# Kernel tuning notes

Measured on AMD Instinct MI355X. Metric: run time of the kernel, lower is better.

Reference implementation:

```python
import jax, jax.numpy as jnp
import numpy as np

ALPHA = 0.99   # config.alpha_grape
GAMMA = 0.999  # config.gamma
LAMBD = 0.7    # config.lambd_grape
T, A = 262144, 64


def setup_inputs() -> dict:
    key = jax.random.key(0)
    ks = jax.random.split(key, 7)
    q = jax.random.normal(ks[0], (T + 1, A), jnp.float32)
    q_tar = jax.random.normal(ks[1], (T + 1, A), jnp.float32)
    # pi / mu are probability distributions over actions (softmax of logits)
    pi = jax.nn.softmax(jax.random.normal(ks[2], (T + 1, A), jnp.float32), axis=-1)
    mu_t = jax.nn.softmax(jax.random.normal(ks[3], (T, A), jnp.float32), axis=-1)
    a_t = jax.random.randint(ks[4], (T,), 0, A, dtype=jnp.int32)
    r_t = jax.random.normal(ks[5], (T,), jnp.float32)
    done_t = jax.random.randint(ks[6], (T,), 0, 2, dtype=jnp.int32)
    return dict(q=q, q_tar=q_tar, pi=pi, a_t=a_t, r_t=r_t, mu_t=mu_t, done_t=done_t)


def reference(q, q_tar, pi, a_t, r_t, mu_t, done_t):
    # GRAPE.compute_targets
    l = q.shape[0] - 1
    idx = jnp.arange(l)
    pi_t, pi_tp1 = pi[:-1], pi[1:]
    q_t, q_tp1 = q[:-1], q_tar[1:]
    q_t_a = q_t[idx, a_t]                              # [T]
    v_t = jnp.sum(pi_t * q_t, axis=1)                  # [T]
    v_tp1 = jnp.sum(pi_tp1 * q_tp1, axis=1)            # [T]
    done_f = done_t.astype(q.dtype)
    q_t_a_est = r_t + (1.0 - done_f) * GAMMA * v_tp1
    td_error = q_t_a_est - q_t_a
    rho_t_a = pi_t[idx, a_t] / mu_t[idx, a_t]
    c_t_a = LAMBD * jnp.clip(rho_t_a, 0.0, 1.0)

    # backward-in-time first-order recurrence over y'
    def step(y_prime, xs):
        est, td, rho, c, d = xs
        y = jnp.where(d > 0.5, 0.0, y_prime)           # reset at episode end
        g = est + y
        y_new = LAMBD * GAMMA * rho * td + GAMMA * c * y
        return y_new, g

    _, g_q = jax.lax.scan(
        step, jnp.float32(0.0),
        (q_t_a_est, td_error, rho_t_a, c_t_a, done_f),
        reverse=True,
    )
    targets_q = g_q + ALPHA * (q_t_a - v_t)            # [T]
    advantages = (1.0 - ALPHA) * (q_t - v_t[:, None])  # [T, A]
    return targets_q, advantages
```

## Files before the change

### kernel.cpp

```cpp
#include <hip/hip_runtime.h>

#define GAMMA 0.999f
#define LAMBD 0.7f
#define ALPHA 0.99f

constexpr int A_DIM = 64;
constexpr int CH    = 128;
constexpr int BLK   = 128;

__global__ __launch_bounds__(BLK, 8)
void k_main(const float* __restrict__ q, const float* __restrict__ q_tar,
            const float* __restrict__ pi, const int* __restrict__ a_t,
            const float* __restrict__ r_t, const float* __restrict__ mu_t,
            const int* __restrict__ done_t,
            float* __restrict__ adv_out,
            float2* __restrict__ comb, float2* __restrict__ cab)
{
    __shared__ float sQa[CH], sRho[CH], sKm[CH], sRt[CH];
    __shared__ float sV[CH], sVp[CH];
    __shared__ float sWA[2], sWB[2];

    const int tid  = threadIdx.x;
    const int wave = tid >> 6, lane = tid & 63;
    const int sub  = lane >> 4, li = lane & 15;
    const int R0   = blockIdx.x * CH;

    {
        int r = R0 + tid;
        int a = a_t[r];
        sRt[tid] = r_t[r];
        sKm[tid] = 1.0f - (float)done_t[r];
        float qa = q[r * A_DIM + a];
        float pa = pi[r * A_DIM + a];
        float ma = mu_t[r * A_DIM + a];
        sQa[tid]  = qa;
        sRho[tid] = pa / ma;
    }

    #pragma unroll 2
    for (int i = 0; i < 8; ++i) {
        int lrowA = wave * 64 + i * 8 + sub;
        int lrowB = lrowA + 4;
        int gA = (R0 + lrowA) * A_DIM + li * 4;
        int gB = (R0 + lrowB) * A_DIM + li * 4;

        float4 piA  = *(const float4*)&pi[gA];
        float4 qA   = *(const float4*)&q[gA];
        float4 pipA = *(const float4*)&pi[gA + A_DIM];
        float4 qpA  = *(const float4*)&q_tar[gA + A_DIM];
        float4 piB  = *(const float4*)&pi[gB];
        float4 qB   = *(const float4*)&q[gB];
        float4 pipB = *(const float4*)&pi[gB + A_DIM];
        float4 qpB  = *(const float4*)&q_tar[gB + A_DIM];

        float s0A = piA.x*qA.x + piA.y*qA.y + piA.z*qA.z + piA.w*qA.w;
        float s1A = pipA.x*qpA.x + pipA.y*qpA.y + pipA.z*qpA.z + pipA.w*qpA.w;
        float s0B = piB.x*qB.x + piB.y*qB.y + piB.z*qB.z + piB.w*qB.w;
        float s1B = pipB.x*qpB.x + pipB.y*qpB.y + pipB.z*qpB.z + pipB.w*qpB.w;
        #pragma unroll
        for (int off = 1; off < 16; off <<= 1) {
            s0A += __shfl_xor(s0A, off);
            s1A += __shfl_xor(s1A, off);
            s0B += __shfl_xor(s0B, off);
            s1B += __shfl_xor(s1B, off);
        }

        float4 advA, advB;
        advA.x = (1.0f - ALPHA) * (qA.x - s0A);
        advA.y = (1.0f - ALPHA) * (qA.y - s0A);
        advA.z = (1.0f - ALPHA) * (qA.z - s0A);
        advA.w = (1.0f - ALPHA) * (qA.w - s0A);
        advB.x = (1.0f - ALPHA) * (qB.x - s0B);
        advB.y = (1.0f - ALPHA) * (qB.y - s0B);
        advB.z = (1.0f - ALPHA) * (qB.z - s0B);
        advB.w = (1.0f - ALPHA) * (qB.w - s0B);
        *(float4*)&adv_out[gA] = advA;
        *(float4*)&adv_out[gB] = advB;

        if (li == 0) {
            sV[lrowA] = s0A;  sVp[lrowA] = s1A;
            sV[lrowB] = s0B;  sVp[lrowB] = s1B;
        }
    }
    __syncthreads();

    float s0    = sV[tid],  s1 = sVp[tid];
    float kmask = sKm[tid];
    float qa    = sQa[tid];
    float rho   = sRho[tid];
    float est = sRt[tid] + kmask * (GAMMA * s1);
    float td  = est - qa;
    float c   = LAMBD * fminf(fmaxf(rho, 0.0f), 1.0f);
    float Fa  = (LAMBD * GAMMA) * rho * td;
    float Fb  = kmask * (GAMMA * c);
    float E   = est + ALPHA * (qa - s0);

    float Ai = Fa, Bi = Fb;
    #pragma unroll
    for (int off = 1; off < 64; off <<= 1) {
        float An = __shfl_down(Ai, off);
        float Bn = __shfl_down(Bi, off);
        if (lane + off < 64) { Ai += Bi * An; Bi *= Bn; }
    }
    if (lane == 0) { sWA[wave] = Ai; sWB[wave] = Bi; }
    float Xa = __shfl_down(Ai, 1);
    float Xb = __shfl_down(Bi, 1);
    if (lane == 63) { Xa = 0.0f; Xb = 1.0f; }
    __syncthreads();
    if (wave == 0) {
        float W1a = sWA[1], W1b = sWB[1];
        Xa = Xa + Xb * W1a;
        Xb = Xb * W1b;
    }
    comb[R0 + tid] = make_float2(E + kmask * Xa, kmask * Xb);
    if (tid == 0) {
        float W1a = sWA[1], W1b = sWB[1];
        cab[blockIdx.x] = make_float2(Ai + Bi * W1a, Bi * W1b);
    }
}

__global__ __launch_bounds__(BLK, 8)
void k_fin(const float2* __restrict__ comb, const float2* __restrict__ cab,
           float* __restrict__ targets, int nch)
{
    __shared__ float sXa[BLK], sXb[BLK];
    __shared__ float sWA[2], sWB[2];
    __shared__ float sYe;
    const int tid = threadIdx.x, bid = blockIdx.x;
    const int wave = tid >> 6, lane = tid & 63;

    const float4* cab4 = (const float4*)cab;
    float A = 0.0f, B = 1.0f;
    #pragma unroll
    for (int j = 0; j < 8; ++j) {
        float4 u = cab4[tid * 8 + j];
        A += B * u.x; B *= u.y;
        A += B * u.z; B *= u.w;
    }

    float Ai = A, Bi = B;
    #pragma unroll
    for (int off = 1; off < 64; off <<= 1) {
        float An = __shfl_down(Ai, off);
        float Bn = __shfl_down(Bi, off);
        if (lane + off < 64) { Ai += Bi * An; Bi *= Bn; }
    }
    if (lane == 0) { sWA[wave] = Ai; sWB[wave] = Bi; }
    float Xa = __shfl_down(Ai, 1);
    float Xb = __shfl_down(Bi, 1);
    if (lane == 63) { Xa = 0.0f; Xb = 1.0f; }
    __syncthreads();
    if (wave == 0) {
        Xa = Xa + Xb * sWA[1];
        Xb = Xb * sWB[1];
    }
    sXa[tid] = Xa; sXb[tid] = Xb;
    __syncthreads();

    if (tid == 0) {
        int c1 = bid + 1;
        float ye;
        if (c1 >= nch) {
            ye = 0.0f;
        } else {
            int jq = c1 >> 4, rq = c1 & 15;
            float Aa = sXa[jq], Bb = sXb[jq];
            for (int k2 = 16 * jq + 15; k2 >= c1; --k2) {
                float2 cv = cab[k2];
                Aa = cv.x + cv.y * Aa;
                Bb = cv.y * Bb;
            }
            ye = Aa;
        }
        sYe = ye;
    }
    __syncthreads();

    float2 uw = comb[bid * CH + tid];
    targets[bid * CH + tid] = uw.x + uw.y * sYe;
}

extern "C" void kernel_launch(void* const* d_in, const int* in_sizes, int n_in,
                              void* d_out, int out_size, void* d_ws, size_t ws_size,
                              hipStream_t stream) {
    const float* q      = (const float*)d_in[0];
    const float* q_tar  = (const float*)d_in[1];
    const float* pi     = (const float*)d_in[2];
    const int*   a_t    = (const int*)  d_in[3];
    const float* r_t    = (const float*)d_in[4];
    const float* mu_t   = (const float*)d_in[5];
    const int*   done_t = (const int*)  d_in[6];

    const int T   = in_sizes[3];
    const int nch = T / CH;

    float* targets = (float*)d_out;
    float* adv     = (float*)d_out + T;

    char* ws = (char*)d_ws;
    float2* comb = (float2*)ws;              ws += (size_t)8 * T;
    float2* cab  = (float2*)ws;

    k_main<<<nch, BLK, 0, stream>>>(q, q_tar, pi, a_t, r_t, mu_t, done_t,
                                    adv, comb, cab);
    k_fin<<<nch, BLK, 0, stream>>>(comb, cab, targets, nch);
}
```

Baseline: 66.52 us.

## Halve chunk size to 64 rows and restructure scan into single-wave blocks

Each k_main block now covers 64 rows instead of 128. The gather loads are split across the two waves, and the per-chunk scan runs in a single wave, which removes the cross-wave shared-memory combine and one barrier. k_fin becomes a one-wave block that processes two chunks per block and scans twice as many chunk carries per lane, using shuffles instead of shared memory. This doubles the number of k_main blocks and the chunk carries, and leaves one wave idle during the scan phase.

```diff
diff --git a/kernel.cpp b/kernel.cpp
--- a/kernel.cpp
+++ b/kernel.cpp
@@ -5,7 +5,7 @@
 #define ALPHA 0.99f
 
 constexpr int A_DIM = 64;
-constexpr int CH    = 128;
+constexpr int CH    = 64;
 constexpr int BLK   = 128;
 
 __global__ __launch_bounds__(BLK, 8)
@@ -16,9 +16,8 @@
             float* __restrict__ adv_out,
             float2* __restrict__ comb, float2* __restrict__ cab)
 {
-    __shared__ float sQa[CH], sRho[CH], sKm[CH], sRt[CH];
+    __shared__ float sQa[CH], sPa[CH], sMa[CH], sKm[CH], sRt[CH];
     __shared__ float sV[CH], sVp[CH];
-    __shared__ float sWA[2], sWB[2];
 
     const int tid  = threadIdx.x;
     const int wave = tid >> 6, lane = tid & 63;
@@ -26,20 +25,21 @@
     const int R0   = blockIdx.x * CH;
 
     {
-        int r = R0 + tid;
+        int r = R0 + lane;
         int a = a_t[r];
-        sRt[tid] = r_t[r];
-        sKm[tid] = 1.0f - (float)done_t[r];
-        float qa = q[r * A_DIM + a];
-        float pa = pi[r * A_DIM + a];
-        float ma = mu_t[r * A_DIM + a];
-        sQa[tid]  = qa;
-        sRho[tid] = pa / ma;
+        if (wave == 0) {
+            sQa[lane] = q[r * A_DIM + a];
+            sPa[lane] = pi[r * A_DIM + a];
+        } else {
+            sMa[lane] = mu_t[r * A_DIM + a];
+            sRt[lane] = r_t[r];
+            sKm[lane] = 1.0f - (float)done_t[r];
+        }
     }
 
     #pragma unroll 2
-    for (int i = 0; i < 8; ++i) {
-        int lrowA = wave * 64 + i * 8 + sub;
+    for (int i = 0; i < 4; ++i) {
+        int lrowA = wave * 32 + i * 8 + sub;
         int lrowB = lrowA + 4;
         int gA = (R0 + lrowA) * A_DIM + li * 4;
         int gB = (R0 + lrowB) * A_DIM + li * 4;
@@ -84,56 +84,44 @@
     }
     __syncthreads();
 
-    float s0    = sV[tid],  s1 = sVp[tid];
-    float kmask = sKm[tid];
-    float qa    = sQa[tid];
-    float rho   = sRho[tid];
-    float est = sRt[tid] + kmask * (GAMMA * s1);
-    float td  = est - qa;
-    float c   = LAMBD * fminf(fmaxf(rho, 0.0f), 1.0f);
-    float Fa  = (LAMBD * GAMMA) * rho * td;
-    float Fb  = kmask * (GAMMA * c);
-    float E   = est + ALPHA * (qa - s0);
+    if (wave == 0) {
+        float s0    = sV[lane],  s1 = sVp[lane];
+        float kmask = sKm[lane];
+        float qa    = sQa[lane];
+        float rho   = sPa[lane] / sMa[lane];
+        float est = sRt[lane] + kmask * (GAMMA * s1);
+        float td  = est - qa;
+        float c   = LAMBD * fminf(fmaxf(rho, 0.0f), 1.0f);
+        float Fa  = (LAMBD * GAMMA) * rho * td;
+        float Fb  = kmask * (GAMMA * c);
+        float E   = est + ALPHA * (qa - s0);
 
-    float Ai = Fa, Bi = Fb;
-    #pragma unroll
-    for (int off = 1; off < 64; off <<= 1) {
-        float An = __shfl_down(Ai, off);
-        float Bn = __shfl_down(Bi, off);
-        if (lane + off < 64) { Ai += Bi * An; Bi *= Bn; }
-    }
-    if (lane == 0) { sWA[wave] = Ai; sWB[wave] = Bi; }
-    float Xa = __shfl_down(Ai, 1);
-    float Xb = __shfl_down(Bi, 1);
-    if (lane == 63) { Xa = 0.0f; Xb = 1.0f; }
-    __syncthreads();
-    if (wave == 0) {
-        float W1a = sWA[1], W1b = sWB[1];
-        Xa = Xa + Xb * W1a;
-        Xb = Xb * W1b;
-    }
-    comb[R0 + tid] = make_float2(E + kmask * Xa, kmask * Xb);
-    if (tid == 0) {
-        float W1a = sWA[1], W1b = sWB[1];
-        cab[blockIdx.x] = make_float2(Ai + Bi * W1a, Bi * W1b);
+        float Ai = Fa, Bi = Fb;
+        #pragma unroll
+        for (int off = 1; off < 64; off <<= 1) {
+            float An = __shfl_down(Ai, off);
+            float Bn = __shfl_down(Bi, off);
+            if (lane + off < 64) { Ai += Bi * An; Bi *= Bn; }
+        }
+        float Xa = __shfl_down(Ai, 1);
+        float Xb = __shfl_down(Bi, 1);
+        if (lane == 63) { Xa = 0.0f; Xb = 1.0f; }
+        comb[R0 + lane] = make_float2(E + kmask * Xa, kmask * Xb);
+        if (lane == 0) cab[blockIdx.x] = make_float2(Ai, Bi);
     }
 }
 
-__global__ __launch_bounds__(BLK, 8)
+__global__ __launch_bounds__(64, 8)
 void k_fin(const float2* __restrict__ comb, const float2* __restrict__ cab,
            float* __restrict__ targets, int nch)
 {
-    __shared__ float sXa[BLK], sXb[BLK];
-    __shared__ float sWA[2], sWB[2];
-    __shared__ float sYe;
-    const int tid = threadIdx.x, bid = blockIdx.x;
-    const int wave = tid >> 6, lane = tid & 63;
+    const int lane = threadIdx.x, bid = blockIdx.x;
 
     const float4* cab4 = (const float4*)cab;
     float A = 0.0f, B = 1.0f;
-    #pragma unroll
-    for (int j = 0; j < 8; ++j) {
-        float4 u = cab4[tid * 8 + j];
+    #pragma unroll 8
+    for (int j = 0; j < 32; ++j) {
+        float4 u = cab4[lane * 32 + j];
         A += B * u.x; B *= u.y;
         A += B * u.z; B *= u.w;
     }
@@ -145,39 +133,34 @@
         float Bn = __shfl_down(Bi, off);
         if (lane + off < 64) { Ai += Bi * An; Bi *= Bn; }
     }
-    if (lane == 0) { sWA[wave] = Ai; sWB[wave] = Bi; }
     float Xa = __shfl_down(Ai, 1);
     float Xb = __shfl_down(Bi, 1);
     if (lane == 63) { Xa = 0.0f; Xb = 1.0f; }
-    __syncthreads();
-    if (wave == 0) {
-        Xa = Xa + Xb * sWA[1];
-        Xb = Xb * sWB[1];
+
+    float ye2;
+    int c1 = 2 * bid + 2;
+    if (c1 >= nch) {
+        ye2 = 0.0f;
+    } else {
+        int jq = c1 >> 6;
+        float Aa = __shfl(Xa, jq);
+        float Bb = __shfl(Xb, jq);
+        int end = jq * 64 + 63;
+        for (int k = end; k >= c1; --k) {
+            float2 cv = cab[k];
+            Aa = cv.x + cv.y * Aa;
+            Bb = cv.y * Bb;
+        }
+        ye2 = Aa;
     }
-    sXa[tid] = Xa; sXb[tid] = Xb;
-    __syncthreads();
+    float2 cm1 = cab[2 * bid + 1];
+    float ye1 = cm1.x + cm1.y * ye2;
 
-    if (tid == 0) {
-        int c1 = bid + 1;
-        float ye;
-        if (c1 >= nch) {
-            ye = 0.0f;
-        } else {
-            int jq = c1 >> 4, rq = c1 & 15;
-            float Aa = sXa[jq], Bb = sXb[jq];
-            for (int k2 = 16 * jq + 15; k2 >= c1; --k2) {
-                float2 cv = cab[k2];
-                Aa = cv.x + cv.y * Aa;
-                Bb = cv.y * Bb;
-            }
-            ye = Aa;
-        }
-        sYe = ye;
-    }
-    __syncthreads();
-
-    float2 uw = comb[bid * CH + tid];
-    targets[bid * CH + tid] = uw.x + uw.y * sYe;
+    int r0 = bid * 128;
+    float2 uw0 = comb[r0 + lane];
+    targets[r0 + lane] = uw0.x + uw0.y * ye1;
+    float2 uw1 = comb[r0 + 64 + lane];
+    targets[r0 + 64 + lane] = uw1.x + uw1.y * ye2;
 }
 
 extern "C" void kernel_launch(void* const* d_in, const int* in_sizes, int n_in,
@@ -203,5 +186,5 @@
 
     k_main<<<nch, BLK, 0, stream>>>(q, q_tar, pi, a_t, r_t, mu_t, done_t,
                                     adv, comb, cab);
-    k_fin<<<nch, BLK, 0, stream>>>(comb, cab, targets, nch);
+    k_fin<<<nch / 2, 64, 0, stream>>>(comb, cab, targets, nch);
 }
```

Measured after the change: 70.79 us. 6.4% more time.

## Double the main-kernel block size, software-prefetch row tiles, use nontemporal stores

Applied to the files above, without the earlier changes.

k_main now runs 256 threads per 128-row chunk. The per-row gather loads for q, pi, mu and the scalars are split across the two thread halves, and each thread handles 4 iterations instead of 8. The row loop explicitly prefetches the next iteration's float4 tiles into registers. The advantage and target outputs are written with nontemporal stores to avoid cache pollution. Only two of the four waves run the scan phase, which leaves the others idle there, and the larger block raises register pressure from the double-buffered tiles.

```diff
diff --git a/kernel.cpp b/kernel.cpp
--- a/kernel.cpp
+++ b/kernel.cpp
@@ -6,9 +6,20 @@
 
 constexpr int A_DIM = 64;
 constexpr int CH    = 128;
-constexpr int BLK   = 128;
-
-__global__ __launch_bounds__(BLK, 8)
+constexpr int BLK   = 256;
+
+typedef float fx4 __attribute__((ext_vector_type(4)));
+
+__device__ __forceinline__ float dot4(const float4& a, const float4& b) {
+    return a.x*b.x + a.y*b.y + a.z*b.z + a.w*b.w;
+}
+
+__device__ __forceinline__ void nt_store4(float* p, float x, float y, float z, float w) {
+    fx4 v = { x, y, z, w };
+    __builtin_nontemporal_store(v, (fx4*)p);
+}
+
+__global__ __launch_bounds__(BLK, 4)
 void k_main(const float* __restrict__ q, const float* __restrict__ q_tar,
             const float* __restrict__ pi, const int* __restrict__ a_t,
             const float* __restrict__ r_t, const float* __restrict__ mu_t,
@@ -16,7 +27,7 @@
             float* __restrict__ adv_out,
             float2* __restrict__ comb, float2* __restrict__ cab)
 {
-    __shared__ float sQa[CH], sRho[CH], sKm[CH], sRt[CH];
+    __shared__ float sQa[CH], sPa[CH], sMa[CH], sKm[CH], sRt[CH];
     __shared__ float sV[CH], sVp[CH];
     __shared__ float sWA[2], sWB[2];
 
@@ -25,38 +36,57 @@
     const int sub  = lane >> 4, li = lane & 15;
     const int R0   = blockIdx.x * CH;
 
-    {
+    if (tid < CH) {
         int r = R0 + tid;
         int a = a_t[r];
-        sRt[tid] = r_t[r];
-        sKm[tid] = 1.0f - (float)done_t[r];
-        float qa = q[r * A_DIM + a];
-        float pa = pi[r * A_DIM + a];
-        float ma = mu_t[r * A_DIM + a];
-        sQa[tid]  = qa;
-        sRho[tid] = pa / ma;
-    }
-
-    #pragma unroll 2
-    for (int i = 0; i < 8; ++i) {
-        int lrowA = wave * 64 + i * 8 + sub;
+        sQa[tid] = q[r * A_DIM + a];
+        sPa[tid] = pi[r * A_DIM + a];
+    } else {
+        int row = tid - CH;
+        int r = R0 + row;
+        int a = a_t[r];
+        sMa[row] = mu_t[r * A_DIM + a];
+        sRt[row] = r_t[r];
+        sKm[row] = 1.0f - (float)done_t[r];
+    }
+
+    const int lrow0 = wave * 32 + sub;
+    float4 piA, qA, pipA, qpA, piB, qB, pipB, qpB;
+    {
+        int gA = (R0 + lrow0) * A_DIM + li * 4;
+        int gB = gA + 4 * A_DIM;
+        piA  = *(const float4*)&pi[gA];
+        qA   = *(const float4*)&q[gA];
+        pipA = *(const float4*)&pi[gA + A_DIM];
+        qpA  = *(const float4*)&q_tar[gA + A_DIM];
+        piB  = *(const float4*)&pi[gB];
+        qB   = *(const float4*)&q[gB];
+        pipB = *(const float4*)&pi[gB + A_DIM];
+        qpB  = *(const float4*)&q_tar[gB + A_DIM];
+    }
+    #pragma unroll
+    for (int i = 0; i < 4; ++i) {
+        float4 npiA, nqA, npipA, nqpA, npiB, nqB, npipB, nqpB;
+        if (i < 3) {
+            int gA = (R0 + lrow0 + (i + 1) * 8) * A_DIM + li * 4;
+            int gB = gA + 4 * A_DIM;
+            npiA  = *(const float4*)&pi[gA];
+            nqA   = *(const float4*)&q[gA];
+            npipA = *(const float4*)&pi[gA + A_DIM];
+            nqpA  = *(const float4*)&q_tar[gA + A_DIM];
+            npiB  = *(const float4*)&pi[gB];
+            nqB   = *(const float4*)&q[gB];
+            npipB = *(const float4*)&pi[gB + A_DIM];
+            nqpB  = *(const float4*)&q_tar[gB + A_DIM];
+        }
+
+        int lrowA = lrow0 + i * 8;
         int lrowB = lrowA + 4;
         int gA = (R0 + lrowA) * A_DIM + li * 4;
         int gB = (R0 + lrowB) * A_DIM + li * 4;
 
-        float4 piA  = *(const float4*)&pi[gA];
-        float4 qA   = *(const float4*)&q[gA];
-        float4 pipA = *(const float4*)&pi[gA + A_DIM];
-        float4 qpA  = *(const float4*)&q_tar[gA + A_DIM];
-        float4 piB  = *(const float4*)&pi[gB];
-        float4 qB   = *(const float4*)&q[gB];
-        float4 pipB = *(const float4*)&pi[gB + A_DIM];
-        float4 qpB  = *(const float4*)&q_tar[gB + A_DIM];
-
-        float s0A = piA.x*qA.x + piA.y*qA.y + piA.z*qA.z + piA.w*qA.w;
-        float s1A = pipA.x*qpA.x + pipA.y*qpA.y + pipA.z*qpA.z + pipA.w*qpA.w;
-        float s0B = piB.x*qB.x + piB.y*qB.y + piB.z*qB.z + piB.w*qB.w;
-        float s1B = pipB.x*qpB.x + pipB.y*qpB.y + pipB.z*qpB.z + pipB.w*qpB.w;
+        float s0A = dot4(piA, qA),  s1A = dot4(pipA, qpA);
+        float s0B = dot4(piB, qB),  s1B = dot4(pipB, qpB);
         #pragma unroll
         for (int off = 1; off < 16; off <<= 1) {
             s0A += __shfl_xor(s0A, off);
@@ -65,65 +95,67 @@
             s1B += __shfl_xor(s1B, off);
         }
 
-        float4 advA, advB;
-        advA.x = (1.0f - ALPHA) * (qA.x - s0A);
-        advA.y = (1.0f - ALPHA) * (qA.y - s0A);
-        advA.z = (1.0f - ALPHA) * (qA.z - s0A);
-        advA.w = (1.0f - ALPHA) * (qA.w - s0A);
-        advB.x = (1.0f - ALPHA) * (qB.x - s0B);
-        advB.y = (1.0f - ALPHA) * (qB.y - s0B);
-        advB.z = (1.0f - ALPHA) * (qB.z - s0B);
-        advB.w = (1.0f - ALPHA) * (qB.w - s0B);
-        *(float4*)&adv_out[gA] = advA;
-        *(float4*)&adv_out[gB] = advB;
+        nt_store4(&adv_out[gA],
+                  (1.0f - ALPHA) * (qA.x - s0A), (1.0f - ALPHA) * (qA.y - s0A),
+                  (1.0f - ALPHA) * (qA.z - s0A), (1.0f - ALPHA) * (qA.w - s0A));
+        nt_store4(&adv_out[gB],
+                  (1.0f - ALPHA) * (qB.x - s0B), (1.0f - ALPHA) * (qB.y - s0B),
+                  (1.0f - ALPHA) * (qB.z - s0B), (1.0f - ALPHA) * (qB.w - s0B));
 
         if (li == 0) {
             sV[lrowA] = s0A;  sVp[lrowA] = s1A;
             sV[lrowB] = s0B;  sVp[lrowB] = s1B;
         }
-    }
-    __syncthreads();
-
-    float s0    = sV[tid],  s1 = sVp[tid];
-    float kmask = sKm[tid];
-    float qa    = sQa[tid];
-    float rho   = sRho[tid];
-    float est = sRt[tid] + kmask * (GAMMA * s1);
-    float td  = est - qa;
-    float c   = LAMBD * fminf(fmaxf(rho, 0.0f), 1.0f);
-    float Fa  = (LAMBD * GAMMA) * rho * td;
-    float Fb  = kmask * (GAMMA * c);
-    float E   = est + ALPHA * (qa - s0);
-
-    float Ai = Fa, Bi = Fb;
-    #pragma unroll
-    for (int off = 1; off < 64; off <<= 1) {
-        float An = __shfl_down(Ai, off);
-        float Bn = __shfl_down(Bi, off);
-        if (lane + off < 64) { Ai += Bi * An; Bi *= Bn; }
-    }
-    if (lane == 0) { sWA[wave] = Ai; sWB[wave] = Bi; }
-    float Xa = __shfl_down(Ai, 1);
-    float Xb = __shfl_down(Bi, 1);
-    if (lane == 63) { Xa = 0.0f; Xb = 1.0f; }
-    __syncthreads();
-    if (wave == 0) {
-        float W1a = sWA[1], W1b = sWB[1];
-        Xa = Xa + Xb * W1a;
-        Xb = Xb * W1b;
-    }
-    comb[R0 + tid] = make_float2(E + kmask * Xa, kmask * Xb);
-    if (tid == 0) {
-        float W1a = sWA[1], W1b = sWB[1];
-        cab[blockIdx.x] = make_float2(Ai + Bi * W1a, Bi * W1b);
-    }
-}
-
-__global__ __launch_bounds__(BLK, 8)
+
+        piA = npiA; qA = nqA; pipA = npipA; qpA = nqpA;
+        piB = npiB; qB = nqB; pipB = npipB; qpB = nqpB;
+    }
+    __syncthreads();
+
+    float Ai = 0.0f, Bi = 1.0f, Xa = 0.0f, Xb = 1.0f;
+    float E = 0.0f, kmask = 0.0f;
+    int   row = wave * 64 + lane;
+    if (wave < 2) {
+        float s0 = sV[row], s1 = sVp[row];
+        kmask = sKm[row];
+        float qa  = sQa[row];
+        float rho = sPa[row] / sMa[row];
+        float est = sRt[row] + kmask * (GAMMA * s1);
+        float td  = est - qa;
+        float c   = LAMBD * fminf(fmaxf(rho, 0.0f), 1.0f);
+        float Fa  = (LAMBD * GAMMA) * rho * td;
+        float Fb  = kmask * (GAMMA * c);
+        E = est + ALPHA * (qa - s0);
+
+        Ai = Fa; Bi = Fb;
+        #pragma unroll
+        for (int off = 1; off < 64; off <<= 1) {
+            float An = __shfl_down(Ai, off);
+            float Bn = __shfl_down(Bi, off);
+            if (lane + off < 64) { Ai += Bi * An; Bi *= Bn; }
+        }
+        if (lane == 0) { sWA[wave] = Ai; sWB[wave] = Bi; }
+        Xa = __shfl_down(Ai, 1);
+        Xb = __shfl_down(Bi, 1);
+        if (lane == 63) { Xa = 0.0f; Xb = 1.0f; }
+    }
+    __syncthreads();
+    if (wave < 2) {
+        if (wave == 0) {
+            Xa = Xa + Xb * sWA[1];
+            Xb = Xb * sWB[1];
+        }
+        comb[R0 + row] = make_float2(E + kmask * Xa, kmask * Xb);
+        if (tid == 0)
+            cab[blockIdx.x] = make_float2(Ai + Bi * sWA[1], Bi * sWB[1]);
+    }
+}
+
+__global__ __launch_bounds__(BLK / 2, 8)
 void k_fin(const float2* __restrict__ comb, const float2* __restrict__ cab,
            float* __restrict__ targets, int nch)
 {
-    __shared__ float sXa[BLK], sXb[BLK];
+    __shared__ float sXa[128], sXb[128];
     __shared__ float sWA[2], sWB[2];
     __shared__ float sYe;
     const int tid = threadIdx.x, bid = blockIdx.x;
@@ -163,7 +195,7 @@
         if (c1 >= nch) {
             ye = 0.0f;
         } else {
-            int jq = c1 >> 4, rq = c1 & 15;
+            int jq = c1 >> 4;
             float Aa = sXa[jq], Bb = sXb[jq];
             for (int k2 = 16 * jq + 15; k2 >= c1; --k2) {
                 float2 cv = cab[k2];
@@ -177,7 +209,7 @@
     __syncthreads();
 
     float2 uw = comb[bid * CH + tid];
-    targets[bid * CH + tid] = uw.x + uw.y * sYe;
+    __builtin_nontemporal_store(uw.x + uw.y * sYe, &targets[bid * CH + tid]);
 }
 
 extern "C" void kernel_launch(void* const* d_in, const int* in_sizes, int n_in,
@@ -203,5 +235,5 @@
 
     k_main<<<nch, BLK, 0, stream>>>(q, q_tar, pi, a_t, r_t, mu_t, done_t,
                                     adv, comb, cab);
-    k_fin<<<nch, BLK, 0, stream>>>(comb, cab, targets, nch);
-}
+    k_fin<<<nch, BLK / 2, 0, stream>>>(comb, cab, targets, nch);
+}
```

Measured after the change: 63.29 us. 4.9% less time.
